# Kernel optimization log

Hardware: AMD Instinct MI355X
Metric: run time of the kernel (lower is better)

Reference implementation:

```python
import jax, jax.numpy as jnp
import numpy as np

B, T, C = 16, 4000, 512
H, K = 8, 31
PAD, STRIDE, DIL = 15, 1, 1


def setup_inputs() -> dict:
    key = jax.random.key(0)
    k1, k2 = jax.random.split(key, 2)
    x = jax.random.normal(k1, (B, T, C), jnp.float32)
    # xavier_uniform on (H, 1, K): fan_in = 1*K, fan_out = 1*K -> limit = sqrt(6/(2K))
    limit = float(np.sqrt(6.0 / (2.0 * K)))
    weights = jax.random.uniform(k2, (H, 1, K), jnp.float32, -limit, limit)
    bias_weights = jnp.zeros((H,), jnp.float32)
    return {"x": x, "weights": weights, "bias_weights": bias_weights}


def reference(x, weights, bias_weights):
    # softmax-normalized per-head kernel (weight_dropout=0 -> eval identity)
    w = jax.nn.softmax(weights, axis=-1)                # (H, 1, K)
    # torch reshape (B,C,T)->(B*C/H, H, T) maps channel c to head c % H;
    # tile replicates heads in exactly that order -> kernel per channel.
    w_full = jnp.tile(w, (C // H, 1, 1))                 # (C, 1, K)
    xc = jnp.transpose(x, (0, 2, 1))                     # (B, C, T)
    out = jax.lax.conv_general_dilated(
        xc, w_full,
        window_strides=(STRIDE,),
        padding=[(PAD, PAD)],
        rhs_dilation=(DIL,),
        feature_group_count=C,
        dimension_numbers=("NCH", "OIH", "NCH"))        # (B, C, T)
    b_full = jnp.tile(bias_weights, C // H)              # (C,) bias per head -> per channel
    out = out + b_full[None, :, None]
    return jnp.transpose(out, (0, 2, 1))                 # (B, T, C)
```

## Files before the change

kernel.cpp:

```cpp
#include <hip/hip_runtime.h>
#include <math.h>


constexpr int NB   = 16;
constexpr int NT   = 4000;
constexpr int NC   = 512;
constexpr int NH   = 8;
constexpr int NK   = 31;
constexpr int CPAD = 15;

constexpr int CH   = 16;
constexpr int HALO = NK - 1;
constexpr int WIN  = CH + HALO;
constexpr int NTC  = NT / CH;
constexpr int NCG  = NC / 256;
constexpr int NWG  = NTC * NCG * NB;
constexpr int NXCD = 8;

__global__ __launch_bounds__(64) void softmax_w_kernel(
    const float* __restrict__ w, float* __restrict__ wn)
{
    const int h = threadIdx.x;
    if (h >= NH) return;
    float v[NK];
    float m = -1e30f;
    #pragma unroll
    for (int k = 0; k < NK; ++k) { v[k] = w[h * NK + k]; m = fmaxf(m, v[k]); }
    float s = 0.0f;
    #pragma unroll
    for (int k = 0; k < NK; ++k) { v[k] = __expf(v[k] - m); s += v[k]; }
    const float inv = 1.0f / s;
    #pragma unroll
    for (int k = 0; k < NK; ++k) wn[h * NK + k] = v[k] * inv;
}

__global__ __launch_bounds__(256, 4) void lconv_kernel(
    const float* __restrict__ x,
    const float* __restrict__ wn,
    const float* __restrict__ bias,
    float* __restrict__ out)
{
    const int orig = blockIdx.x;
    const int lin  = (orig % NXCD) * (NWG / NXCD) + orig / NXCD;
    const int tc   = lin % NTC;
    const int rest = lin / NTC;
    const int cg   = rest % NCG;
    const int b    = rest / NCG;

    const int c  = cg * 256 + threadIdx.x;
    const int t0 = tc * CH;
    const int h  = c & (NH - 1);

    const float* xb = x   + (size_t)b * NT * NC + c;
    float*       ob = out + (size_t)b * NT * NC + c;

    float wr[NK];
    #pragma unroll
    for (int k = 0; k < NK; ++k) wr[k] = wn[h * NK + k];
    const float bv = bias[h];

    float win[WIN];
    if (t0 >= CPAD && t0 + CH - 1 + CPAD < NT) {
        #pragma unroll
        for (int i = 0; i < WIN; ++i)
            win[i] = xb[(size_t)(t0 - CPAD + i) * NC];
    } else {
        #pragma unroll
        for (int i = 0; i < WIN; ++i) {
            const int t = t0 - CPAD + i;
            win[i] = (t >= 0 && t < NT) ? xb[(size_t)t * NC] : 0.0f;
        }
    }

    __builtin_amdgcn_sched_barrier(0);

    #pragma unroll
    for (int j = 0; j < CH; ++j) {
        float acc = bv;
        #pragma unroll
        for (int k = 0; k < NK; ++k) acc = fmaf(win[j + k], wr[k], acc);
        ob[(size_t)(t0 + j) * NC] = acc;
    }
}

extern "C" void kernel_launch(void* const* d_in, const int* in_sizes, int n_in,
                              void* d_out, int out_size, void* d_ws, size_t ws_size,
                              hipStream_t stream) {
    const float* x    = (const float*)d_in[0];
    const float* w    = (const float*)d_in[1];
    const float* bias = (const float*)d_in[2];
    float*       out  = (float*)d_out;
    float*       wnrm = (float*)d_ws;

    softmax_w_kernel<<<1, 64, 0, stream>>>(w, wnrm);
    lconv_kernel<<<NWG, 256, 0, stream>>>(x, wnrm, bias, out);
}
```

Before: 241.2 us.

## Stage input window through LDS with direct global-to-LDS 16-byte loads

```diff
diff --git a/kernel.cpp b/kernel.cpp
--- a/kernel.cpp
+++ b/kernel.cpp
@@ -9,13 +9,13 @@
 constexpr int NK   = 31;
 constexpr int CPAD = 15;
 
-constexpr int CH   = 16;
-constexpr int HALO = NK - 1;
-constexpr int WIN  = CH + HALO;
-constexpr int NTC  = NT / CH;
-constexpr int NCG  = NC / 256;
-constexpr int NWG  = NTC * NCG * NB;
-constexpr int NXCD = 8;
+constexpr int CH    = 16;
+constexpr int WIN   = CH + NK - 1;
+constexpr int ROWS4 = 48;
+constexpr int NTC   = NT / CH;
+constexpr int NCG   = NC / 256;
+constexpr int NWG   = NTC * NCG * NB;
+constexpr int NXCD  = 8;
 
 __global__ __launch_bounds__(64) void softmax_w_kernel(
     const float* __restrict__ w, float* __restrict__ wn)
@@ -34,12 +34,14 @@
     for (int k = 0; k < NK; ++k) wn[h * NK + k] = v[k] * inv;
 }
 
-__global__ __launch_bounds__(256, 4) void lconv_kernel(
+__global__ __launch_bounds__(256, 3) void lconv_kernel(
     const float* __restrict__ x,
     const float* __restrict__ wn,
     const float* __restrict__ bias,
     float* __restrict__ out)
 {
+    __shared__ float tile[4 * ROWS4 * 64];
+
     const int orig = blockIdx.x;
     const int lin  = (orig % NXCD) * (NWG / NXCD) + orig / NXCD;
     const int tc   = lin % NTC;
@@ -47,40 +49,71 @@
     const int cg   = rest % NCG;
     const int b    = rest / NCG;
 
-    const int c  = cg * 256 + threadIdx.x;
-    const int t0 = tc * CH;
-    const int h  = c & (NH - 1);
+    const int tid   = threadIdx.x;
+    const int wv    = tid >> 6;
+    const int ln    = tid & 63;
+    const int c     = cg * 256 + tid;
+    const int h     = c & (NH - 1);
+    const int t0    = tc * CH;
+    const int cbase = cg * 256 + wv * 64;
 
-    const float* xb = x   + (size_t)b * NT * NC + c;
-    float*       ob = out + (size_t)b * NT * NC + c;
+    float* wtile = &tile[wv * (ROWS4 * 64)];
+    const float* xg = x + (size_t)b * NT * NC;
+
+    if (tc >= 1 && tc <= NTC - 3) {
+        #pragma unroll
+        for (int i = 0; i < ROWS4 / 4; ++i) {
+            const int t = t0 - CPAD + 4 * i + (ln >> 4);
+            const float* g = xg + (size_t)t * NC + cbase + (ln & 15) * 4;
+            __builtin_amdgcn_global_load_lds(
+                (const __attribute__((address_space(1))) void*)g,
+                (__attribute__((address_space(3))) void*)&wtile[i * 256],
+                16, 0, 0);
+        }
+    } else {
+        #pragma unroll 1
+        for (int r = 0; r < WIN; ++r) {
+            const int t = t0 - CPAD + r;
+            float* dst = &wtile[(r >> 2) * 256 + (r & 3) * 64];
+            if (t >= 0 && t < NT) {
+                const float* g = xg + (size_t)t * NC + cbase + ln;
+                __builtin_amdgcn_global_load_lds(
+                    (const __attribute__((address_space(1))) void*)g,
+                    (__attribute__((address_space(3))) void*)dst,
+                    4, 0, 0);
+            } else {
+                dst[ln] = 0.0f;
+            }
+        }
+    }
 
     float wr[NK];
     #pragma unroll
     for (int k = 0; k < NK; ++k) wr[k] = wn[h * NK + k];
     const float bv = bias[h];
 
-    float win[WIN];
-    if (t0 >= CPAD && t0 + CH - 1 + CPAD < NT) {
+    __builtin_amdgcn_s_waitcnt(0x0F70);
+    __builtin_amdgcn_sched_barrier(0);
+
+    float acc[CH];
+    #pragma unroll
+    for (int j = 0; j < CH; ++j) acc[j] = bv;
+
+    #pragma unroll
+    for (int r = 0; r < WIN; ++r) {
+        const float v = wtile[(r >> 2) * 256 + (r & 3) * 64 + ln];
         #pragma unroll
-        for (int i = 0; i < WIN; ++i)
-            win[i] = xb[(size_t)(t0 - CPAD + i) * NC];
-    } else {
-        #pragma unroll
-        for (int i = 0; i < WIN; ++i) {
-            const int t = t0 - CPAD + i;
-            win[i] = (t >= 0 && t < NT) ? xb[(size_t)t * NC] : 0.0f;
+        for (int j = 0; j < CH; ++j) {
+            const int k = r - j;
+            if (k >= 0 && k < NK)
+                acc[j] = fmaf(v, wr[k], acc[j]);
         }
     }
 
-    __builtin_amdgcn_sched_barrier(0);
-
+    float* ob = out + (size_t)b * NT * NC + c;
     #pragma unroll
-    for (int j = 0; j < CH; ++j) {
-        float acc = bv;
-        #pragma unroll
-        for (int k = 0; k < NK; ++k) acc = fmaf(win[j + k], wr[k], acc);
-        ob[(size_t)(t0 + j) * NC] = acc;
-    }
+    for (int j = 0; j < CH; ++j)
+        ob[(size_t)(t0 + j) * NC] = acc[j];
 }
 
 extern "C" void kernel_launch(void* const* d_in, const int* in_sizes, int n_in,
```

New measurement: 242.0 us. About the same (+0.3%).
